# Performance work log

Hardware: AMD Instinct MI355X
Metric: run time of the kernel (lower is better)

Reference implementation:

```python
import jax, jax.numpy as jnp
import numpy as np

# pywt 'db4' decomposition low-pass filter (L = 8 taps)
_DEC_LO = np.array([
    -0.010597401784997278, 0.032883011666982945, 0.030841381835986965,
    -0.18703481171888114, -0.02798376941698385, 0.6308807679295904,
    0.7148465705525415, 0.23037781330885523], dtype=np.float32)
# pywt convention: dec_hi[n] = (-1)^(n+1) * dec_lo[L-1-n]
_SIGNS = np.array([-1.0, 1.0] * 4, dtype=np.float32)
_DEC_HI = _DEC_LO[::-1].copy() * _SIGNS

DEC_LO = jnp.asarray(_DEC_LO)
DEC_HI = jnp.asarray(_DEC_HI)
LEVELS = 3


def _dwt_per(x):
    """One level of periodization-mode DWT along axis 1.

    x: (B, N, F) with N even. Returns (cA, cD), each (B, N//2, F).
    Matches pywt: c[k] = sum_j f[j] * x[(2k + 1 - j) mod N].
    """
    N = x.shape[1]
    L = DEC_LO.shape[0]
    k = jnp.arange(N // 2)
    j = jnp.arange(L)
    idx = (2 * k[:, None] + 1 - j[None, :]) % N          # (N//2, L)
    g = x[:, idx, :]                                      # (B, N//2, L, F)
    cA = jnp.einsum('bklf,l->bkf', g, DEC_LO)
    cD = jnp.einsum('bklf,l->bkf', g, DEC_HI)
    return cA, cD


def reference(x):
    """Multilevel db4 wavedec (periodization) along axis -2 of (B, N, F).

    Returns the flat coefficient tensor (B, K, F) with pywt ordering
    [cA_L, cD_L, cD_{L-1}, ..., cD_1] concatenated along axis 1.
    """
    a = x
    details = []
    for _ in range(LEVELS):
        a, d = _dwt_per(a)
        details.append(d)
    return jnp.concatenate([a] + details[::-1], axis=1)


def setup_inputs() -> dict:
    key = jax.random.key(0)
    x = jax.random.normal(key, (64, 4096, 64), dtype=jnp.float32)
    return {"x": x}


if __name__ == "__main__":
    out = reference(**setup_inputs())
    print(out.shape)
```

## Files before the change

### kernel.cpp

```cpp
#include <hip/hip_runtime.h>


__global__ __launch_bounds__(256) void dwt3_fused(
    const float* __restrict__ in,
    float* __restrict__ out)
{
    const float LOR[8] = { 0.23037781330885523f,   0.7148465705525415f,
                           0.6308807679295904f,   -0.02798376941698385f,
                          -0.18703481171888114f,   0.030841381835986965f,
                           0.032883011666982945f, -0.010597401784997278f};
    const float HIR[8] = {-0.010597401784997278f, -0.032883011666982945f,
                           0.030841381835986965f,  0.18703481171888114f,
                          -0.02798376941698385f,  -0.6308807679295904f,
                           0.7148465705525415f,   -0.23037781330885523f};

    const int f    = threadIdx.x & 63;
    const int wv   = threadIdx.x >> 6;
    const int b    = blockIdx.x >> 4;
    const int tile = (blockIdx.x & 15) * 4 + wv;
    const int K3   = tile * 8;

    const float* inB  = in  + (size_t)b * 4096 * 64 + f;
    float*       outB = out + (size_t)b * 4096 * 64 + f;

    const int i1s = 4 * K3 - 18;

    float w0[8];
    float w1[8] = {0,0,0,0,0,0,0,0};
    float w2[8] = {0,0,0,0,0,0,0,0};

    #pragma unroll
    for (int m = 0; m < 8; ++m) {
        const int r = (2 * i1s - 6 + m) & 4095;
        w0[m] = inB[r * 64];
    }

    #pragma unroll
    for (int s = 0; s < 50; ++s) {
        const int i1 = i1s + s;
        if (s > 0) {
            #pragma unroll
            for (int m = 0; m < 6; ++m) w0[m] = w0[m + 2];
            const int ra = (2 * i1)     & 4095;
            const int rb = (2 * i1 + 1) & 4095;
            w0[6] = inB[ra * 64];
            w0[7] = inB[rb * 64];
        }

        float a1 = 0.f;
        #pragma unroll
        for (int m = 0; m < 8; ++m) a1 = fmaf(w0[m], LOR[m], a1);
        if (s >= 18) {
            float d1 = 0.f;
            #pragma unroll
            for (int m = 0; m < 8; ++m) d1 = fmaf(w0[m], HIR[m], d1);
            outB[(size_t)((2048 + i1) & 4095) * 64] = d1;
        }
        #pragma unroll
        for (int m = 0; m < 7; ++m) w1[m] = w1[m + 1];
        w1[7] = a1;

        if ((s & 1) && s >= 7) {
            const int i2 = 2 * K3 + (s - 19) / 2;
            float a2 = 0.f;
            #pragma unroll
            for (int m = 0; m < 8; ++m) a2 = fmaf(w1[m], LOR[m], a2);
            if (s >= 19) {
                float d2 = 0.f;
                #pragma unroll
                for (int m = 0; m < 8; ++m) d2 = fmaf(w1[m], HIR[m], d2);
                outB[(size_t)((1024 + i2) & 4095) * 64] = d2;
            }
            #pragma unroll
            for (int m = 0; m < 7; ++m) w2[m] = w2[m + 1];
            w2[7] = a2;

            if (s >= 21 && ((s - 21) & 3) == 0) {
                const int i3 = K3 + (s - 21) / 4;
                float a3 = 0.f, d3 = 0.f;
                #pragma unroll
                for (int m = 0; m < 8; ++m) {
                    a3 = fmaf(w2[m], LOR[m], a3);
                    d3 = fmaf(w2[m], HIR[m], d3);
                }
                outB[(size_t)(i3 & 4095) * 64]           = a3;
                outB[(size_t)((512 + i3) & 4095) * 64]   = d3;
            }
        }
    }
}

extern "C" void kernel_launch(void* const* d_in, const int* in_sizes, int n_in,
                              void* d_out, int out_size, void* d_ws, size_t ws_size,
                              hipStream_t stream) {
    (void)in_sizes; (void)n_in; (void)out_size; (void)d_ws; (void)ws_size;
    const float* x = (const float*)d_in[0];
    float* out = (float*)d_out;
    dwt3_fused<<<1024, 256, 0, stream>>>(x, out);
}
```

Before: 116.5 us.

## Process two features per thread with float2 loads and swizzled block mapping

Result: no change. 115.7 us (-0.7%).

```diff
diff --git a/kernel.cpp b/kernel.cpp
--- a/kernel.cpp
+++ b/kernel.cpp
@@ -1,7 +1,19 @@
 #include <hip/hip_runtime.h>
 
 
-__global__ __launch_bounds__(256) void dwt3_fused(
+__device__ __forceinline__ float2 ld2(const float* p) {
+    return *reinterpret_cast<const float2*>(p);
+}
+__device__ __forceinline__ void st2(float* p, float2 v) {
+    *reinterpret_cast<float2*>(p) = v;
+}
+__device__ __forceinline__ float2 fma2(float2 a, float s, float2 c) {
+    c.x = fmaf(a.x, s, c.x);
+    c.y = fmaf(a.y, s, c.y);
+    return c;
+}
+
+__global__ __launch_bounds__(256) void dwt3_fused_v2(
     const float* __restrict__ in,
     float* __restrict__ out)
 {
@@ -14,10 +26,15 @@
                           -0.02798376941698385f,  -0.6308807679295904f,
                            0.7148465705525415f,   -0.23037781330885523f};
 
-    const int f    = threadIdx.x & 63;
+    const int bid  = blockIdx.x;
+    const int swz  = (bid & 7) * 64 + (bid >> 3);
+
+    const int lane = threadIdx.x & 63;
     const int wv   = threadIdx.x >> 6;
-    const int b    = blockIdx.x >> 4;
-    const int tile = (blockIdx.x & 15) * 4 + wv;
+    const int f    = (lane & 31) * 2;
+    const int tsub = lane >> 5;
+    const int b    = swz >> 3;
+    const int tile = (swz & 7) * 8 + wv * 2 + tsub;
     const int K3   = tile * 8;
 
     const float* inB  = in  + (size_t)b * 4096 * 64 + f;
@@ -25,14 +42,19 @@
 
     const int i1s = 4 * K3 - 18;
 
-    float w0[8];
-    float w1[8] = {0,0,0,0,0,0,0,0};
-    float w2[8] = {0,0,0,0,0,0,0,0};
+    float2 w0[8];
+    float2 w1[8];
+    float2 w2[8];
+    #pragma unroll
+    for (int m = 0; m < 8; ++m) {
+        w1[m] = make_float2(0.f, 0.f);
+        w2[m] = make_float2(0.f, 0.f);
+    }
 
     #pragma unroll
     for (int m = 0; m < 8; ++m) {
         const int r = (2 * i1s - 6 + m) & 4095;
-        w0[m] = inB[r * 64];
+        w0[m] = ld2(inB + (size_t)r * 64);
     }
 
     #pragma unroll
@@ -43,18 +65,18 @@
             for (int m = 0; m < 6; ++m) w0[m] = w0[m + 2];
             const int ra = (2 * i1)     & 4095;
             const int rb = (2 * i1 + 1) & 4095;
-            w0[6] = inB[ra * 64];
-            w0[7] = inB[rb * 64];
+            w0[6] = ld2(inB + (size_t)ra * 64);
+            w0[7] = ld2(inB + (size_t)rb * 64);
         }
 
-        float a1 = 0.f;
+        float2 a1 = make_float2(0.f, 0.f);
         #pragma unroll
-        for (int m = 0; m < 8; ++m) a1 = fmaf(w0[m], LOR[m], a1);
+        for (int m = 0; m < 8; ++m) a1 = fma2(w0[m], LOR[m], a1);
         if (s >= 18) {
-            float d1 = 0.f;
+            float2 d1 = make_float2(0.f, 0.f);
             #pragma unroll
-            for (int m = 0; m < 8; ++m) d1 = fmaf(w0[m], HIR[m], d1);
-            outB[(size_t)((2048 + i1) & 4095) * 64] = d1;
+            for (int m = 0; m < 8; ++m) d1 = fma2(w0[m], HIR[m], d1);
+            st2(outB + (size_t)((2048 + i1) & 4095) * 64, d1);
         }
         #pragma unroll
         for (int m = 0; m < 7; ++m) w1[m] = w1[m + 1];
@@ -62,14 +84,14 @@
 
         if ((s & 1) && s >= 7) {
             const int i2 = 2 * K3 + (s - 19) / 2;
-            float a2 = 0.f;
+            float2 a2 = make_float2(0.f, 0.f);
             #pragma unroll
-            for (int m = 0; m < 8; ++m) a2 = fmaf(w1[m], LOR[m], a2);
+            for (int m = 0; m < 8; ++m) a2 = fma2(w1[m], LOR[m], a2);
             if (s >= 19) {
-                float d2 = 0.f;
+                float2 d2 = make_float2(0.f, 0.f);
                 #pragma unroll
-                for (int m = 0; m < 8; ++m) d2 = fmaf(w1[m], HIR[m], d2);
-                outB[(size_t)((1024 + i2) & 4095) * 64] = d2;
+                for (int m = 0; m < 8; ++m) d2 = fma2(w1[m], HIR[m], d2);
+                st2(outB + (size_t)((1024 + i2) & 4095) * 64, d2);
             }
             #pragma unroll
             for (int m = 0; m < 7; ++m) w2[m] = w2[m + 1];
@@ -77,14 +99,15 @@
 
             if (s >= 21 && ((s - 21) & 3) == 0) {
                 const int i3 = K3 + (s - 21) / 4;
-                float a3 = 0.f, d3 = 0.f;
+                float2 a3 = make_float2(0.f, 0.f);
+                float2 d3 = make_float2(0.f, 0.f);
                 #pragma unroll
                 for (int m = 0; m < 8; ++m) {
-                    a3 = fmaf(w2[m], LOR[m], a3);
-                    d3 = fmaf(w2[m], HIR[m], d3);
+                    a3 = fma2(w2[m], LOR[m], a3);
+                    d3 = fma2(w2[m], HIR[m], d3);
                 }
-                outB[(size_t)(i3 & 4095) * 64]           = a3;
-                outB[(size_t)((512 + i3) & 4095) * 64]   = d3;
+                st2(outB + (size_t)(i3 & 4095) * 64,         a3);
+                st2(outB + (size_t)((512 + i3) & 4095) * 64, d3);
             }
         }
     }
@@ -96,5 +119,5 @@
     (void)in_sizes; (void)n_in; (void)out_size; (void)d_ws; (void)ws_size;
     const float* x = (const float*)d_in[0];
     float* out = (float*)d_out;
-    dwt3_fused<<<1024, 256, 0, stream>>>(x, out);
+    dwt3_fused_v2<<<512, 256, 0, stream>>>(x, out);
 }
```
